# Kernel optimization log

Measured on AMD Instinct MI355X. Metric: run time of the kernel, lower is better.

## Reference

```python
import jax, jax.numpy as jnp
import numpy as np

LOG2 = float(np.log(2.0))

def ssp(x):
    # shifted softplus: log(0.5*exp(x) + 0.5)
    return jax.nn.softplus(x) - LOG2


def setup_inputs() -> dict:
    B, A, N = 8, 512, 64
    n_atom, n_spatial, n_filters = 256, 128, 256
    n_ang_feat = 2 * 2 * 2 * 8 * 2  # 2*n_zetas*2*n_angular*n_zetas = 128
    key = jax.random.key(0)
    ks = jax.random.split(key, 16)
    f32 = jnp.float32
    inp = {
        'x': jax.random.normal(ks[0], (B, A, n_atom), f32),
        'r_ij': jax.random.uniform(ks[1], (B, A, N), f32) * 6.0,  # some beyond cutoff=5
        'f_ij': jax.random.normal(ks[2], (B, A, N, n_spatial), f32),
        'G_i': jax.random.normal(ks[3], (B, A, n_ang_feat), f32),
        'neighbor_mask': jnp.ones((B, A, N), f32),
        'neighbors': jax.random.randint(ks[4], (B, A, N), 0, A),
        # CFConv params: in2f (no bias), filter MLP, f2out
        'W_in2f': jax.random.normal(ks[5], (n_atom, n_filters), f32) * (n_atom ** -0.5),
        'W1': jax.random.normal(ks[6], (n_spatial, n_filters), f32) * (n_spatial ** -0.5),
        'b1': jnp.zeros((n_filters,), f32),
        'W2': jax.random.normal(ks[7], (n_filters, n_filters), f32) * (n_filters ** -0.5),
        'b2': jnp.zeros((n_filters,), f32),
        'W_f2out': jax.random.normal(ks[8], (n_filters, n_atom), f32) * (n_filters ** -0.5),
        'b_f2out': jnp.zeros((n_atom,), f32),
        # post-cfconv dense and angular dense (no bias)
        'W_dense': jax.random.normal(ks[9], (n_atom, n_atom), f32) * (n_atom ** -0.5),
        'b_dense': jnp.zeros((n_atom,), f32),
        'W_ang': jax.random.normal(ks[10], (n_ang_feat, n_atom), f32) * (n_ang_feat ** -0.5),
    }
    return inp


def reference(x, r_ij, f_ij, G_i, neighbor_mask, neighbors,
              W_in2f, W1, b1, W2, b2, W_f2out, b_f2out,
              W_dense, b_dense, W_ang):
    cutoff = 5.0
    # filter-generating MLP on distance expansion: [B,A,N,n_filters]
    W = ssp(jnp.einsum('bans,sf->banf', f_ij, W1) + b1)
    W = jnp.einsum('banf,fg->bang', W, W2) + b2
    # hard cutoff mask on distances
    C = (r_ij <= cutoff).astype(W.dtype)
    W = W * C[..., None]
    # in2f projection then neighbor gather
    xf = jnp.einsum('bad,df->baf', x, W_in2f)  # [B,A,F]
    B, A, F = xf.shape
    N = neighbors.shape[-1]
    y = jnp.take_along_axis(xf, neighbors.reshape(B, A * N, 1), axis=1)
    y = y.reshape(B, A, N, F)
    # elementwise filter, mask padded neighbors, sum-aggregate over neighbors
    y = (y * W * neighbor_mask[..., None]).sum(axis=2)  # [B,A,F]
    v_rad = jnp.einsum('baf,fd->bad', y, W_f2out) + b_f2out
    v_rad = jnp.einsum('bad,de->bae', v_rad, W_dense) + b_dense
    v_ang = jnp.einsum('bag,gd->bad', G_i, W_ang)
    return ssp(v_rad + v_ang)
```

## Files before the change

kernel.cpp:

```cpp
#include <hip/hip_runtime.h>


typedef __bf16 bf16x8 __attribute__((ext_vector_type(8)));
typedef __bf16 bf16x2 __attribute__((ext_vector_type(2)));
typedef float f32x4 __attribute__((ext_vector_type(4)));
typedef int i32x4 __attribute__((ext_vector_type(4)));
typedef unsigned short u16;
typedef unsigned int u32;

#define LDA 136
#define LDH 264

static __device__ __forceinline__ float b2f(u16 u) {
  union { float f; u32 i; } v; v.i = ((u32)u) << 16; return v.f;
}
static __device__ __forceinline__ u16 f2b(float f) {
  return __builtin_bit_cast(u16, (__bf16)f);
}
static __device__ __forceinline__ u32 pk2(float lo, float hi) {
  bf16x2 v; v[0] = (__bf16)lo; v[1] = (__bf16)hi;
  return __builtin_bit_cast(u32, v);
}
static __device__ __forceinline__ float sspf(float x) {
  float t = __expf(fminf(x, 60.0f));
  return __logf(fmaf(t, 0.5f, 0.5f));
}
static __device__ __forceinline__ bf16x8 ldfrag(const u16* p) {
  return __builtin_bit_cast(bf16x8, *(const uint4*)p);
}
static __device__ __forceinline__ float ldsc(const u16* p, bool fm, size_t i) {
  return fm ? ((const float*)p)[i] : b2f(p[i]);
}

static __device__ __forceinline__ void pack_strip(
    const u16* __restrict__ W, bool fm, int q, int KC, u16* __restrict__ dst, u16* T) {
  int tid = threadIdx.x;
  if (fm) {
    const float* src = (const float*)W + (size_t)q * 32 * 256;
#pragma unroll
    for (int i = 0; i < 8; i++) {
      int c = tid + 256 * i;
      int row = c >> 6, col4 = (c & 63) * 4;
      float4 v = *(const float4*)(src + (size_t)row * 256 + col4);
      uint2 o; o.x = pk2(v.x, v.y); o.y = pk2(v.z, v.w);
      *(uint2*)(T + row * LDH + col4) = o;
    }
  } else {
    const u16* src = W + (size_t)q * 32 * 256;
#pragma unroll
    for (int i = 0; i < 8; i++) {
      int c = tid + 256 * i;
      int row = c >> 6, col4 = (c & 63) * 4;
      *(uint2*)(T + row * LDH + col4) = *(const uint2*)(src + (size_t)row * 256 + col4);
    }
  }
  __syncthreads();
#pragma unroll
  for (int i = 0; i < 4; i++) {
    int idx = tid + 256 * i;
    int flane = idx & 63, c = idx >> 6;
    int col = c * 16 + (flane & 15);
    int r0 = (flane >> 4) * 8;
    u32 t0 = (u32)T[(r0 + 0) * LDH + col] | ((u32)T[(r0 + 1) * LDH + col] << 16);
    u32 t1 = (u32)T[(r0 + 2) * LDH + col] | ((u32)T[(r0 + 3) * LDH + col] << 16);
    u32 t2 = (u32)T[(r0 + 4) * LDH + col] | ((u32)T[(r0 + 5) * LDH + col] << 16);
    u32 t3 = (u32)T[(r0 + 6) * LDH + col] | ((u32)T[(r0 + 7) * LDH + col] << 16);
    uint4 o; o.x = t0; o.y = t1; o.z = t2; o.w = t3;
    *(uint4*)(dst + ((size_t)(c * KC + q) * 64 + flane) * 8) = o;
  }
}

__global__ __launch_bounds__(256) void pack_a(
    const u16* __restrict__ Win, const u16* __restrict__ W1, const u16* __restrict__ W2,
    const u16* __restrict__ nm, u16* __restrict__ outb) {
  __shared__ __align__(16) u16 T[32 * LDH];
  bool fm = (nm[0] == 0);
  int b = blockIdx.x;
  if (b < 8)       pack_strip(Win, fm, b,      8, outb + 1048576, T);
  else if (b < 12) pack_strip(W1,  fm, b - 8,  4, outb + 1114112, T);
  else             pack_strip(W2,  fm, b - 12, 8, outb + 1146880, T);
}

__global__ __launch_bounds__(256) void pack_b(
    const u16* __restrict__ Wf, const u16* __restrict__ Wd, const u16* __restrict__ Wa,
    const u16* __restrict__ nm, u16* __restrict__ dst) {
  __shared__ __align__(16) u16 T[32 * LDH];
  bool fm = (nm[0] == 0);
  int b = blockIdx.x;
  if (b < 8)       pack_strip(Wf, fm, b,      8, dst + 98304,  T);
  else if (b < 16) pack_strip(Wd, fm, b - 8,  8, dst + 163840, T);
  else             pack_strip(Wa, fm, b - 16, 4, dst + 229376, T);
}

__global__ __launch_bounds__(256) void k1_xf(
    const u16* __restrict__ x, const u16* __restrict__ nm, u16* __restrict__ outb) {
  __shared__ __align__(16) u16 sX[16 * LDH];
  bool fm = (nm[0] == 0);
  int bid = blockIdx.x, tid = threadIdx.x;
  int w = tid >> 6, lane = tid & 63, quad = lane >> 4, l16 = lane & 15;
  if (fm) {
    const float* src = (const float*)x + (size_t)bid * 4096;
#pragma unroll
    for (int i = 0; i < 2; i++) {
      int c = tid + 256 * i;
      float4 a = *(const float4*)(src + c * 8), b = *(const float4*)(src + c * 8 + 4);
      uint4 o; o.x = pk2(a.x, a.y); o.y = pk2(a.z, a.w);
      o.z = pk2(b.x, b.y); o.w = pk2(b.z, b.w);
      *(uint4*)(sX + (c >> 5) * LDH + (c & 31) * 8) = o;
    }
  } else {
    const u16* src = x + (size_t)bid * 4096;
#pragma unroll
    for (int i = 0; i < 2; i++) {
      int c = tid + 256 * i;
      *(uint4*)(sX + (c >> 5) * LDH + (c & 31) * 8) = *(const uint4*)(src + c * 8);
    }
  }
  __syncthreads();
  const u16* winp = outb + 1048576;
  f32x4 acc[4];
#pragma unroll
  for (int ct = 0; ct < 4; ct++) acc[ct] = (f32x4){0.f, 0.f, 0.f, 0.f};
#pragma unroll
  for (int q = 0; q < 8; q++) {
    bf16x8 af = ldfrag(sX + l16 * LDH + q * 32 + quad * 8);
    bf16x8 bfr[4];
#pragma unroll
    for (int ct = 0; ct < 4; ct++)
      bfr[ct] = ldfrag(winp + ((size_t)((w * 4 + ct) * 8 + q) * 64 + lane) * 8);
#pragma unroll
    for (int ct = 0; ct < 4; ct++)
      acc[ct] = __builtin_amdgcn_mfma_f32_16x16x32_bf16(af, bfr[ct], acc[ct], 0, 0, 0);
  }
#pragma unroll
  for (int ct = 0; ct < 4; ct++) {
    int f = w * 64 + ct * 16 + l16;
#pragma unroll
    for (int r = 0; r < 4; r++)
      outb[(size_t)(bid * 16 + quad * 4 + r) * 256 + f] = f2b(acc[ct][r]);
  }
}

__global__ __launch_bounds__(256, 3) void k2_main(
    u16* __restrict__ fij, const u16* __restrict__ rij, const u16* __restrict__ nm,
    const int* __restrict__ nbr, const u16* __restrict__ b1, const u16* __restrict__ b2,
    const u16* __restrict__ xf) {
  __shared__ __align__(16) u16 sF[64 * LDA];
  __shared__ __align__(16) u16 sH[64 * LDH];
  __shared__ __align__(16) float cm[64];
  __shared__ __align__(16) int nb[64];
  bool fm = (nm[0] == 0);
  const u16* w1p = xf + 1114112;
  const u16* w2p = xf + 1146880;
  int bid = blockIdx.x, tid = threadIdx.x;
  int w = tid >> 6, lane = tid & 63, quad = lane >> 4, l16 = lane & 15;

  if (fm) {
    const float* fsrc = (const float*)fij + (size_t)bid * 8192;
#pragma unroll
    for (int i = 0; i < 4; i++) {
      int c = tid + 256 * i;
      const float* p = fsrc + c * 8;
      float4 a = *(const float4*)p, b = *(const float4*)(p + 4);
      uint4 o; o.x = pk2(a.x, a.y); o.y = pk2(a.z, a.w);
      o.z = pk2(b.x, b.y); o.w = pk2(b.z, b.w);
      *(uint4*)(sF + (c >> 4) * LDA + (c & 15) * 8) = o;
    }
  } else {
    const u16* fsrc = fij + (size_t)bid * 8192;
#pragma unroll
    for (int i = 0; i < 4; i++) {
      int c = tid + 256 * i;
      *(uint4*)(sF + (c >> 4) * LDA + (c & 15) * 8) = *(const uint4*)(fsrc + c * 8);
    }
  }
  if (tid < 64) {
    float r = ldsc(rij, fm, (size_t)bid * 64 + tid);
    float m = ldsc(nm, fm, (size_t)bid * 64 + tid);
    cm[tid] = (r <= 5.0f) ? m : 0.0f;
    nb[tid] = nbr[bid * 64 + tid];
  }
  __syncthreads();

  f32x4 zero = {0.f, 0.f, 0.f, 0.f};
  f32x4 acc[4][4];
#pragma unroll
  for (int mt = 0; mt < 4; mt++)
#pragma unroll
    for (int ct = 0; ct < 4; ct++) acc[mt][ct] = zero;
#pragma unroll
  for (int q = 0; q < 4; q++) {
    bf16x8 af[4], bfr[4];
#pragma unroll
    for (int mt = 0; mt < 4; mt++)
      af[mt] = ldfrag(sF + (mt * 16 + l16) * LDA + q * 32 + quad * 8);
#pragma unroll
    for (int ct = 0; ct < 4; ct++)
      bfr[ct] = ldfrag(w1p + ((size_t)((w * 4 + ct) * 4 + q) * 64 + lane) * 8);
#pragma unroll
    for (int mt = 0; mt < 4; mt++)
#pragma unroll
      for (int ct = 0; ct < 4; ct++)
        acc[mt][ct] = __builtin_amdgcn_mfma_f32_16x16x32_bf16(af[mt], bfr[ct], acc[mt][ct], 0, 0, 0);
  }
  float bb1[4];
#pragma unroll
  for (int ct = 0; ct < 4; ct++) bb1[ct] = ldsc(b1, fm, w * 64 + ct * 16 + l16);
#pragma unroll
  for (int ct = 0; ct < 4; ct++) {
    int f = w * 64 + ct * 16 + l16;
#pragma unroll
    for (int mt = 0; mt < 4; mt++)
#pragma unroll
      for (int r = 0; r < 4; r++)
        sH[(mt * 16 + quad * 4 + r) * LDH + f] = f2b(sspf(acc[mt][ct][r] + bb1[ct]));
  }
  __syncthreads();

  f32x4 acc2[4][4];
#pragma unroll
  for (int mt = 0; mt < 4; mt++)
#pragma unroll
    for (int ct = 0; ct < 4; ct++) acc2[mt][ct] = zero;
#pragma unroll 2
  for (int q = 0; q < 8; q++) {
    bf16x8 af[4], bfr[4];
#pragma unroll
    for (int mt = 0; mt < 4; mt++)
      af[mt] = ldfrag(sH + (mt * 16 + l16) * LDH + q * 32 + quad * 8);
#pragma unroll
    for (int ct = 0; ct < 4; ct++)
      bfr[ct] = ldfrag(w2p + ((size_t)((w * 4 + ct) * 8 + q) * 64 + lane) * 8);
#pragma unroll
    for (int mt = 0; mt < 4; mt++)
#pragma unroll
      for (int ct = 0; ct < 4; ct++)
        acc2[mt][ct] = __builtin_amdgcn_mfma_f32_16x16x32_bf16(af[mt], bfr[ct], acc2[mt][ct], 0, 0, 0);
  }

  float bb2[4];
#pragma unroll
  for (int ct = 0; ct < 4; ct++) bb2[ct] = ldsc(b2, fm, w * 64 + ct * 16 + l16);
  int b_of = (bid >> 9) * 512;
  float s[4] = {0.f, 0.f, 0.f, 0.f};
#pragma unroll
  for (int mt = 0; mt < 4; mt++) {
    f32x4 cmv = *(const f32x4*)(cm + mt * 16 + quad * 4);
    i32x4 nbv = *(const i32x4*)(nb + mt * 16 + quad * 4);
#pragma unroll
    for (int r = 0; r < 4; r++) {
      const u16* xrow = xf + (size_t)(b_of + nbv[r]) * 256 + w * 64 + l16;
      float c = cmv[r];
#pragma unroll
      for (int ct = 0; ct < 4; ct++)
        s[ct] = fmaf((acc2[mt][ct][r] + bb2[ct]) * c, b2f(xrow[ct * 16]), s[ct]);
    }
  }
#pragma unroll
  for (int ct = 0; ct < 4; ct++) {
    s[ct] += __shfl_xor(s[ct], 16);
    s[ct] += __shfl_xor(s[ct], 32);
  }
  if (quad == 0) {
    size_t yoff = (size_t)bid * (fm ? 16384 : 8192);
#pragma unroll
    for (int ct = 0; ct < 4; ct++)
      fij[yoff + w * 64 + ct * 16 + l16] = f2b(s[ct]);
  }
}

__global__ __launch_bounds__(256, 3) void k3_out(
    const u16* __restrict__ fij, const u16* __restrict__ G, const u16* __restrict__ bf2,
    const u16* __restrict__ bd, const u16* __restrict__ nm,
    const u16* __restrict__ packed, u16* __restrict__ outb) {
  __shared__ __align__(16) u16 sY[32 * LDH];
  __shared__ __align__(16) u16 sH2[32 * LDH];
  __shared__ __align__(16) u16 sG[32 * LDA];
  bool fm = (nm[0] == 0);
  const u16* wfp = packed + 98304;
  const u16* wdp = packed + 163840;
  const u16* wap = packed + 229376;
  int bid = blockIdx.x, tid = threadIdx.x;
  int w = tid >> 6, lane = tid & 63, quad = lane >> 4, l16 = lane & 15;
  size_t ystr = fm ? 16384 : 8192;
#pragma unroll
  for (int i = 0; i < 4; i++) {
    int c = tid + 256 * i;
    int row = c >> 5;
    const u16* src = fij + (size_t)(bid * 32 + row) * ystr + (c & 31) * 8;
    *(uint4*)(sY + row * LDH + (c & 31) * 8) = *(const uint4*)src;
  }
  if (fm) {
    const float* g32 = (const float*)G;
#pragma unroll
    for (int i = 0; i < 2; i++) {
      int c = tid + 256 * i;
      int row = c >> 4;
      const float* p = g32 + (size_t)(bid * 32 + row) * 128 + (c & 15) * 8;
      float4 a = *(const float4*)p, b = *(const float4*)(p + 4);
      uint4 o; o.x = pk2(a.x, a.y); o.y = pk2(a.z, a.w);
      o.z = pk2(b.x, b.y); o.w = pk2(b.z, b.w);
      *(uint4*)(sG + row * LDA + (c & 15) * 8) = o;
    }
  } else {
#pragma unroll
    for (int i = 0; i < 2; i++) {
      int c = tid + 256 * i;
      int row = c >> 4;
      *(uint4*)(sG + row * LDA + (c & 15) * 8) =
          *(const uint4*)(G + (size_t)(bid * 32 + row) * 128 + (c & 15) * 8);
    }
  }
  __syncthreads();
  f32x4 zero = {0.f, 0.f, 0.f, 0.f};
  f32x4 acc[2][4];
#pragma unroll
  for (int mt = 0; mt < 2; mt++)
#pragma unroll
    for (int ct = 0; ct < 4; ct++) acc[mt][ct] = zero;
#pragma unroll
  for (int q = 0; q < 8; q++) {
    bf16x8 af[2], bfr[4];
#pragma unroll
    for (int mt = 0; mt < 2; mt++)
      af[mt] = ldfrag(sY + (mt * 16 + l16) * LDH + q * 32 + quad * 8);
#pragma unroll
    for (int ct = 0; ct < 4; ct++)
      bfr[ct] = ldfrag(wfp + ((size_t)((w * 4 + ct) * 8 + q) * 64 + lane) * 8);
#pragma unroll
    for (int mt = 0; mt < 2; mt++)
#pragma unroll
      for (int ct = 0; ct < 4; ct++)
        acc[mt][ct] = __builtin_amdgcn_mfma_f32_16x16x32_bf16(af[mt], bfr[ct], acc[mt][ct], 0, 0, 0);
  }
#pragma unroll
  for (int ct = 0; ct < 4; ct++) {
    int f = w * 64 + ct * 16 + l16;
    float bb = ldsc(bf2, fm, f);
#pragma unroll
    for (int mt = 0; mt < 2; mt++)
#pragma unroll
      for (int r = 0; r < 4; r++)
        sH2[(mt * 16 + quad * 4 + r) * LDH + f] = f2b(acc[mt][ct][r] + bb);
  }
  __syncthreads();
#pragma unroll
  for (int mt = 0; mt < 2; mt++)
#pragma unroll
    for (int ct = 0; ct < 4; ct++) acc[mt][ct] = zero;
#pragma unroll
  for (int q = 0; q < 8; q++) {
    bf16x8 af[2], bfr[4];
#pragma unroll
    for (int mt = 0; mt < 2; mt++)
      af[mt] = ldfrag(sH2 + (mt * 16 + l16) * LDH + q * 32 + quad * 8);
#pragma unroll
    for (int ct = 0; ct < 4; ct++)
      bfr[ct] = ldfrag(wdp + ((size_t)((w * 4 + ct) * 8 + q) * 64 + lane) * 8);
#pragma unroll
    for (int mt = 0; mt < 2; mt++)
#pragma unroll
      for (int ct = 0; ct < 4; ct++)
        acc[mt][ct] = __builtin_amdgcn_mfma_f32_16x16x32_bf16(af[mt], bfr[ct], acc[mt][ct], 0, 0, 0);
  }
#pragma unroll
  for (int q = 0; q < 4; q++) {
    bf16x8 af[2], bfr[4];
#pragma unroll
    for (int mt = 0; mt < 2; mt++)
      af[mt] = ldfrag(sG + (mt * 16 + l16) * LDA + q * 32 + quad * 8);
#pragma unroll
    for (int ct = 0; ct < 4; ct++)
      bfr[ct] = ldfrag(wap + ((size_t)((w * 4 + ct) * 4 + q) * 64 + lane) * 8);
#pragma unroll
    for (int mt = 0; mt < 2; mt++)
#pragma unroll
      for (int ct = 0; ct < 4; ct++)
        acc[mt][ct] = __builtin_amdgcn_mfma_f32_16x16x32_bf16(af[mt], bfr[ct], acc[mt][ct], 0, 0, 0);
  }
  float* out32 = (float*)outb;
#pragma unroll
  for (int ct = 0; ct < 4; ct++) {
    int f = w * 64 + ct * 16 + l16;
    float bb = ldsc(bd, fm, f);
#pragma unroll
    for (int mt = 0; mt < 2; mt++)
#pragma unroll
      for (int r = 0; r < 4; r++) {
        int m = mt * 16 + quad * 4 + r;
        float v = sspf(acc[mt][ct][r] + bb);
        size_t idx = ((size_t)bid * 32 + m) * 256 + f;
        if (fm) out32[idx] = v; else outb[idx] = f2b(v);
      }
  }
}

extern "C" void kernel_launch(void* const* d_in, const int* in_sizes, int n_in,
                              void* d_out, int out_size, void* d_ws, size_t ws_size,
                              hipStream_t stream) {
  u16*       x    = (u16*)d_in[0];
  const u16* rij  = (const u16*)d_in[1];
  u16*       fij  = (u16*)d_in[2];
  const u16* Gi   = (const u16*)d_in[3];
  const u16* nmsk = (const u16*)d_in[4];
  const int* nbr  = (const int*)d_in[5];
  const u16* Win  = (const u16*)d_in[6];
  const u16* W1   = (const u16*)d_in[7];
  const u16* b1   = (const u16*)d_in[8];
  const u16* W2   = (const u16*)d_in[9];
  const u16* b2   = (const u16*)d_in[10];
  const u16* Wf   = (const u16*)d_in[11];
  const u16* bf2  = (const u16*)d_in[12];
  const u16* Wd   = (const u16*)d_in[13];
  const u16* bd   = (const u16*)d_in[14];
  const u16* Wa   = (const u16*)d_in[15];
  u16* out = (u16*)d_out;

  pack_a<<<20, 256, 0, stream>>>(Win, W1, W2, nmsk, out);
  k1_xf<<<256, 256, 0, stream>>>(x, nmsk, out);
  pack_b<<<20, 256, 0, stream>>>(Wf, Wd, Wa, nmsk, x);
  k2_main<<<4096, 256, 0, stream>>>(fij, rij, nmsk, nbr, b1, b2, out);
  k3_out<<<128, 256, 0, stream>>>(fij, Gi, bf2, bd, nmsk, x, out);
}
```

Baseline: 293.6 us.

## Permute packed weight columns for vectorized stores and gathers; alias LDS; retile k1/k3

Packed weight fragments now use a column permutation, so each lane owns four adjacent output features. Epilogues can then write packed uint2 stores, and the neighbor gather of xf loads 8 bytes at once instead of four scalar bf16 loads. k2 aliases the f_ij and hidden LDS buffers to cut shared memory and raises the occupancy hint to 4 blocks. An extra barrier is added to make the aliasing safe. k1 and k3 are retiled into smaller row blocks with more blocks and threads for better parallelism.

```diff
diff --git a/kernel.cpp b/kernel.cpp
--- a/kernel.cpp
+++ b/kernel.cpp
@@ -14,6 +14,12 @@
 static __device__ __forceinline__ float b2f(u16 u) {
   union { float f; u32 i; } v; v.i = ((u32)u) << 16; return v.f;
 }
+static __device__ __forceinline__ float b2f_lo(u32 p) {
+  union { float f; u32 i; } v; v.i = p << 16; return v.f;
+}
+static __device__ __forceinline__ float b2f_hi(u32 p) {
+  union { float f; u32 i; } v; v.i = p & 0xffff0000u; return v.f;
+}
 static __device__ __forceinline__ u16 f2b(float f) {
   return __builtin_bit_cast(u16, (__bf16)f);
 }
@@ -59,7 +65,7 @@
   for (int i = 0; i < 4; i++) {
     int idx = tid + 256 * i;
     int flane = idx & 63, c = idx >> 6;
-    int col = c * 16 + (flane & 15);
+    int col = (c >> 2) * 64 + (flane & 15) * 4 + (c & 3);
     int r0 = (flane >> 4) * 8;
     u32 t0 = (u32)T[(r0 + 0) * LDH + col] | ((u32)T[(r0 + 1) * LDH + col] << 16);
     u32 t1 = (u32)T[(r0 + 2) * LDH + col] | ((u32)T[(r0 + 3) * LDH + col] << 16);
@@ -99,22 +105,16 @@
   int bid = blockIdx.x, tid = threadIdx.x;
   int w = tid >> 6, lane = tid & 63, quad = lane >> 4, l16 = lane & 15;
   if (fm) {
-    const float* src = (const float*)x + (size_t)bid * 4096;
-#pragma unroll
-    for (int i = 0; i < 2; i++) {
-      int c = tid + 256 * i;
-      float4 a = *(const float4*)(src + c * 8), b = *(const float4*)(src + c * 8 + 4);
-      uint4 o; o.x = pk2(a.x, a.y); o.y = pk2(a.z, a.w);
-      o.z = pk2(b.x, b.y); o.w = pk2(b.z, b.w);
-      *(uint4*)(sX + (c >> 5) * LDH + (c & 31) * 8) = o;
-    }
-  } else {
-    const u16* src = x + (size_t)bid * 4096;
-#pragma unroll
-    for (int i = 0; i < 2; i++) {
-      int c = tid + 256 * i;
-      *(uint4*)(sX + (c >> 5) * LDH + (c & 31) * 8) = *(const uint4*)(src + c * 8);
-    }
+    const float* src = (const float*)x + (size_t)bid * 2048;
+    int c = tid;
+    float4 a = *(const float4*)(src + c * 8), b = *(const float4*)(src + c * 8 + 4);
+    uint4 o; o.x = pk2(a.x, a.y); o.y = pk2(a.z, a.w);
+    o.z = pk2(b.x, b.y); o.w = pk2(b.z, b.w);
+    *(uint4*)(sX + (c >> 5) * LDH + (c & 31) * 8) = o;
+  } else {
+    const u16* src = x + (size_t)bid * 2048;
+    int c = tid;
+    *(uint4*)(sX + (c >> 5) * LDH + (c & 31) * 8) = *(const uint4*)(src + c * 8);
   }
   __syncthreads();
   const u16* winp = outb + 1048576;
@@ -132,26 +132,28 @@
     for (int ct = 0; ct < 4; ct++)
       acc[ct] = __builtin_amdgcn_mfma_f32_16x16x32_bf16(af, bfr[ct], acc[ct], 0, 0, 0);
   }
-#pragma unroll
-  for (int ct = 0; ct < 4; ct++) {
-    int f = w * 64 + ct * 16 + l16;
-#pragma unroll
-    for (int r = 0; r < 4; r++)
-      outb[(size_t)(bid * 16 + quad * 4 + r) * 256 + f] = f2b(acc[ct][r]);
-  }
-}
-
-__global__ __launch_bounds__(256, 3) void k2_main(
+  if (quad < 2) {
+#pragma unroll
+    for (int r = 0; r < 4; r++) {
+      uint2 o; o.x = pk2(acc[0][r], acc[1][r]); o.y = pk2(acc[2][r], acc[3][r]);
+      *(uint2*)(outb + (size_t)(bid * 8 + quad * 4 + r) * 256 + w * 64 + l16 * 4) = o;
+    }
+  }
+}
+
+__global__ __launch_bounds__(256, 4) void k2_main(
     u16* __restrict__ fij, const u16* __restrict__ rij, const u16* __restrict__ nm,
     const int* __restrict__ nbr, const u16* __restrict__ b1, const u16* __restrict__ b2,
-    const u16* __restrict__ xf) {
-  __shared__ __align__(16) u16 sF[64 * LDA];
-  __shared__ __align__(16) u16 sH[64 * LDH];
+    const u16* __restrict__ outb) {
+  __shared__ __align__(16) u16 sU[64 * LDH];
   __shared__ __align__(16) float cm[64];
   __shared__ __align__(16) int nb[64];
+  u16* sF = sU;
+  u16* sH = sU;
   bool fm = (nm[0] == 0);
-  const u16* w1p = xf + 1114112;
-  const u16* w2p = xf + 1146880;
+  const u16* xf  = outb;
+  const u16* w1p = outb + 1114112;
+  const u16* w2p = outb + 1146880;
   int bid = blockIdx.x, tid = threadIdx.x;
   int w = tid >> 6, lane = tid & 63, quad = lane >> 4, l16 = lane & 15;
 
@@ -203,18 +205,26 @@
       for (int ct = 0; ct < 4; ct++)
         acc[mt][ct] = __builtin_amdgcn_mfma_f32_16x16x32_bf16(af[mt], bfr[ct], acc[mt][ct], 0, 0, 0);
   }
+  __syncthreads();
+
   float bb1[4];
-#pragma unroll
-  for (int ct = 0; ct < 4; ct++) bb1[ct] = ldsc(b1, fm, w * 64 + ct * 16 + l16);
-#pragma unroll
-  for (int ct = 0; ct < 4; ct++) {
-    int f = w * 64 + ct * 16 + l16;
-#pragma unroll
-    for (int mt = 0; mt < 4; mt++)
-#pragma unroll
-      for (int r = 0; r < 4; r++)
-        sH[(mt * 16 + quad * 4 + r) * LDH + f] = f2b(sspf(acc[mt][ct][r] + bb1[ct]));
-  }
+  if (fm) {
+    float4 t = *(const float4*)((const float*)b1 + w * 64 + l16 * 4);
+    bb1[0] = t.x; bb1[1] = t.y; bb1[2] = t.z; bb1[3] = t.w;
+  } else {
+    uint2 t = *(const uint2*)(b1 + w * 64 + l16 * 4);
+    bb1[0] = b2f_lo(t.x); bb1[1] = b2f_hi(t.x); bb1[2] = b2f_lo(t.y); bb1[3] = b2f_hi(t.y);
+  }
+#pragma unroll
+  for (int mt = 0; mt < 4; mt++)
+#pragma unroll
+    for (int r = 0; r < 4; r++) {
+      int m = mt * 16 + quad * 4 + r;
+      uint2 o;
+      o.x = pk2(sspf(acc[mt][0][r] + bb1[0]), sspf(acc[mt][1][r] + bb1[1]));
+      o.y = pk2(sspf(acc[mt][2][r] + bb1[2]), sspf(acc[mt][3][r] + bb1[3]));
+      *(uint2*)(sH + m * LDH + w * 64 + l16 * 4) = o;
+    }
   __syncthreads();
 
   f32x4 acc2[4][4];
@@ -239,159 +249,149 @@
   }
 
   float bb2[4];
-#pragma unroll
-  for (int ct = 0; ct < 4; ct++) bb2[ct] = ldsc(b2, fm, w * 64 + ct * 16 + l16);
+  if (fm) {
+    float4 t = *(const float4*)((const float*)b2 + w * 64 + l16 * 4);
+    bb2[0] = t.x; bb2[1] = t.y; bb2[2] = t.z; bb2[3] = t.w;
+  } else {
+    uint2 t = *(const uint2*)(b2 + w * 64 + l16 * 4);
+    bb2[0] = b2f_lo(t.x); bb2[1] = b2f_hi(t.x); bb2[2] = b2f_lo(t.y); bb2[3] = b2f_hi(t.y);
+  }
   int b_of = (bid >> 9) * 512;
-  float s[4] = {0.f, 0.f, 0.f, 0.f};
+  const u16* xcol = xf + w * 64 + l16 * 4;
+  float s0 = 0.f, s1 = 0.f, s2 = 0.f, s3 = 0.f;
 #pragma unroll
   for (int mt = 0; mt < 4; mt++) {
     f32x4 cmv = *(const f32x4*)(cm + mt * 16 + quad * 4);
     i32x4 nbv = *(const i32x4*)(nb + mt * 16 + quad * 4);
 #pragma unroll
     for (int r = 0; r < 4; r++) {
-      const u16* xrow = xf + (size_t)(b_of + nbv[r]) * 256 + w * 64 + l16;
+      uint2 xv = *(const uint2*)(xcol + (size_t)(b_of + nbv[r]) * 256);
       float c = cmv[r];
-#pragma unroll
-      for (int ct = 0; ct < 4; ct++)
-        s[ct] = fmaf((acc2[mt][ct][r] + bb2[ct]) * c, b2f(xrow[ct * 16]), s[ct]);
-    }
-  }
-#pragma unroll
-  for (int ct = 0; ct < 4; ct++) {
-    s[ct] += __shfl_xor(s[ct], 16);
-    s[ct] += __shfl_xor(s[ct], 32);
-  }
+      s0 = fmaf((acc2[mt][0][r] + bb2[0]) * c, b2f_lo(xv.x), s0);
+      s1 = fmaf((acc2[mt][1][r] + bb2[1]) * c, b2f_hi(xv.x), s1);
+      s2 = fmaf((acc2[mt][2][r] + bb2[2]) * c, b2f_lo(xv.y), s2);
+      s3 = fmaf((acc2[mt][3][r] + bb2[3]) * c, b2f_hi(xv.y), s3);
+    }
+  }
+  s0 += __shfl_xor(s0, 16); s0 += __shfl_xor(s0, 32);
+  s1 += __shfl_xor(s1, 16); s1 += __shfl_xor(s1, 32);
+  s2 += __shfl_xor(s2, 16); s2 += __shfl_xor(s2, 32);
+  s3 += __shfl_xor(s3, 16); s3 += __shfl_xor(s3, 32);
   if (quad == 0) {
     size_t yoff = (size_t)bid * (fm ? 16384 : 8192);
-#pragma unroll
-    for (int ct = 0; ct < 4; ct++)
-      fij[yoff + w * 64 + ct * 16 + l16] = f2b(s[ct]);
-  }
-}
-
-__global__ __launch_bounds__(256, 3) void k3_out(
+    uint2 o; o.x = pk2(s0, s1); o.y = pk2(s2, s3);
+    *(uint2*)(fij + yoff + w * 64 + l16 * 4) = o;
+  }
+}
+
+__global__ __launch_bounds__(512) void k3_out(
     const u16* __restrict__ fij, const u16* __restrict__ G, const u16* __restrict__ bf2,
     const u16* __restrict__ bd, const u16* __restrict__ nm,
     const u16* __restrict__ packed, u16* __restrict__ outb) {
-  __shared__ __align__(16) u16 sY[32 * LDH];
-  __shared__ __align__(16) u16 sH2[32 * LDH];
-  __shared__ __align__(16) u16 sG[32 * LDA];
+  __shared__ __align__(16) u16 sY[16 * LDH];
+  __shared__ __align__(16) u16 sH2[16 * LDH];
+  __shared__ __align__(16) u16 sG[16 * LDA];
   bool fm = (nm[0] == 0);
   const u16* wfp = packed + 98304;
   const u16* wdp = packed + 163840;
   const u16* wap = packed + 229376;
   int bid = blockIdx.x, tid = threadIdx.x;
-  int w = tid >> 6, lane = tid & 63, quad = lane >> 4, l16 = lane & 15;
+  int cg = tid >> 6, lane = tid & 63, quad = lane >> 4, l16 = lane & 15;
+  int f0 = (cg >> 1) * 64 + l16 * 4 + (cg & 1) * 2;
   size_t ystr = fm ? 16384 : 8192;
-#pragma unroll
-  for (int i = 0; i < 4; i++) {
-    int c = tid + 256 * i;
-    int row = c >> 5;
-    const u16* src = fij + (size_t)(bid * 32 + row) * ystr + (c & 31) * 8;
-    *(uint4*)(sY + row * LDH + (c & 31) * 8) = *(const uint4*)src;
-  }
-  if (fm) {
-    const float* g32 = (const float*)G;
-#pragma unroll
-    for (int i = 0; i < 2; i++) {
-      int c = tid + 256 * i;
-      int row = c >> 4;
-      const float* p = g32 + (size_t)(bid * 32 + row) * 128 + (c & 15) * 8;
+  {
+    int c = tid;
+    const u16* src = fij + (size_t)(bid * 16 + (c >> 5)) * ystr + (c & 31) * 8;
+    *(uint4*)(sY + (c >> 5) * LDH + (c & 31) * 8) = *(const uint4*)src;
+  }
+  if (fm) {
+    if (tid < 256) {
+      int c = tid;
+      const float* p = (const float*)G + (size_t)(bid * 16 + (c >> 4)) * 128 + (c & 15) * 8;
       float4 a = *(const float4*)p, b = *(const float4*)(p + 4);
       uint4 o; o.x = pk2(a.x, a.y); o.y = pk2(a.z, a.w);
       o.z = pk2(b.x, b.y); o.w = pk2(b.z, b.w);
-      *(uint4*)(sG + row * LDA + (c & 15) * 8) = o;
-    }
-  } else {
-#pragma unroll
-    for (int i = 0; i < 2; i++) {
-      int c = tid + 256 * i;
-      int row = c >> 4;
-      *(uint4*)(sG + row * LDA + (c & 15) * 8) =
-          *(const uint4*)(G + (size_t)(bid * 32 + row) * 128 + (c & 15) * 8);
+      *(uint4*)(sG + (c >> 4) * LDA + (c & 15) * 8) = o;
+    }
+  } else {
+    if (tid < 256) {
+      int c = tid;
+      *(uint4*)(sG + (c >> 4) * LDA + (c & 15) * 8) =
+          *(const uint4*)(G + (size_t)(bid * 16 + (c >> 4)) * 128 + (c & 15) * 8);
     }
   }
   __syncthreads();
   f32x4 zero = {0.f, 0.f, 0.f, 0.f};
-  f32x4 acc[2][4];
-#pragma unroll
-  for (int mt = 0; mt < 2; mt++)
-#pragma unroll
-    for (int ct = 0; ct < 4; ct++) acc[mt][ct] = zero;
+  f32x4 acc[2];
+  acc[0] = zero; acc[1] = zero;
 #pragma unroll
   for (int q = 0; q < 8; q++) {
-    bf16x8 af[2], bfr[4];
-#pragma unroll
-    for (int mt = 0; mt < 2; mt++)
-      af[mt] = ldfrag(sY + (mt * 16 + l16) * LDH + q * 32 + quad * 8);
-#pragma unroll
-    for (int ct = 0; ct < 4; ct++)
-      bfr[ct] = ldfrag(wfp + ((size_t)((w * 4 + ct) * 8 + q) * 64 + lane) * 8);
-#pragma unroll
-    for (int mt = 0; mt < 2; mt++)
-#pragma unroll
-      for (int ct = 0; ct < 4; ct++)
-        acc[mt][ct] = __builtin_amdgcn_mfma_f32_16x16x32_bf16(af[mt], bfr[ct], acc[mt][ct], 0, 0, 0);
-  }
-#pragma unroll
-  for (int ct = 0; ct < 4; ct++) {
-    int f = w * 64 + ct * 16 + l16;
-    float bb = ldsc(bf2, fm, f);
-#pragma unroll
-    for (int mt = 0; mt < 2; mt++)
-#pragma unroll
-      for (int r = 0; r < 4; r++)
-        sH2[(mt * 16 + quad * 4 + r) * LDH + f] = f2b(acc[mt][ct][r] + bb);
-  }
-  __syncthreads();
-#pragma unroll
-  for (int mt = 0; mt < 2; mt++)
-#pragma unroll
-    for (int ct = 0; ct < 4; ct++) acc[mt][ct] = zero;
+    bf16x8 af = ldfrag(sY + l16 * LDH + q * 32 + quad * 8);
+    bf16x8 bfr[2];
+#pragma unroll
+    for (int ct = 0; ct < 2; ct++)
+      bfr[ct] = ldfrag(wfp + ((size_t)((cg * 2 + ct) * 8 + q) * 64 + lane) * 8);
+#pragma unroll
+    for (int ct = 0; ct < 2; ct++)
+      acc[ct] = __builtin_amdgcn_mfma_f32_16x16x32_bf16(af, bfr[ct], acc[ct], 0, 0, 0);
+  }
+  float bm0, bm1;
+  if (fm) {
+    float2 t = *(const float2*)((const float*)bf2 + f0);
+    bm0 = t.x; bm1 = t.y;
+  } else {
+    u32 t = *(const u32*)(bf2 + f0);
+    bm0 = b2f_lo(t); bm1 = b2f_hi(t);
+  }
+#pragma unroll
+  for (int r = 0; r < 4; r++) {
+    int m = quad * 4 + r;
+    *(u32*)(sH2 + m * LDH + f0) = pk2(acc[0][r] + bm0, acc[1][r] + bm1);
+  }
+  __syncthreads();
+  acc[0] = zero; acc[1] = zero;
 #pragma unroll
   for (int q = 0; q < 8; q++) {
-    bf16x8 af[2], bfr[4];
-#pragma unroll
-    for (int mt = 0; mt < 2; mt++)
-      af[mt] = ldfrag(sH2 + (mt * 16 + l16) * LDH + q * 32 + quad * 8);
-#pragma unroll
-    for (int ct = 0; ct < 4; ct++)
-      bfr[ct] = ldfrag(wdp + ((size_t)((w * 4 + ct) * 8 + q) * 64 + lane) * 8);
-#pragma unroll
-    for (int mt = 0; mt < 2; mt++)
-#pragma unroll
-      for (int ct = 0; ct < 4; ct++)
-        acc[mt][ct] = __builtin_amdgcn_mfma_f32_16x16x32_bf16(af[mt], bfr[ct], acc[mt][ct], 0, 0, 0);
+    bf16x8 af = ldfrag(sH2 + l16 * LDH + q * 32 + quad * 8);
+    bf16x8 bfr[2];
+#pragma unroll
+    for (int ct = 0; ct < 2; ct++)
+      bfr[ct] = ldfrag(wdp + ((size_t)((cg * 2 + ct) * 8 + q) * 64 + lane) * 8);
+#pragma unroll
+    for (int ct = 0; ct < 2; ct++)
+      acc[ct] = __builtin_amdgcn_mfma_f32_16x16x32_bf16(af, bfr[ct], acc[ct], 0, 0, 0);
   }
 #pragma unroll
   for (int q = 0; q < 4; q++) {
-    bf16x8 af[2], bfr[4];
-#pragma unroll
-    for (int mt = 0; mt < 2; mt++)
-      af[mt] = ldfrag(sG + (mt * 16 + l16) * LDA + q * 32 + quad * 8);
-#pragma unroll
-    for (int ct = 0; ct < 4; ct++)
-      bfr[ct] = ldfrag(wap + ((size_t)((w * 4 + ct) * 4 + q) * 64 + lane) * 8);
-#pragma unroll
-    for (int mt = 0; mt < 2; mt++)
-#pragma unroll
-      for (int ct = 0; ct < 4; ct++)
-        acc[mt][ct] = __builtin_amdgcn_mfma_f32_16x16x32_bf16(af[mt], bfr[ct], acc[mt][ct], 0, 0, 0);
+    bf16x8 af = ldfrag(sG + l16 * LDA + q * 32 + quad * 8);
+    bf16x8 bfr[2];
+#pragma unroll
+    for (int ct = 0; ct < 2; ct++)
+      bfr[ct] = ldfrag(wap + ((size_t)((cg * 2 + ct) * 4 + q) * 64 + lane) * 8);
+#pragma unroll
+    for (int ct = 0; ct < 2; ct++)
+      acc[ct] = __builtin_amdgcn_mfma_f32_16x16x32_bf16(af, bfr[ct], acc[ct], 0, 0, 0);
+  }
+  float bd0, bd1;
+  if (fm) {
+    float2 t = *(const float2*)((const float*)bd + f0);
+    bd0 = t.x; bd1 = t.y;
+  } else {
+    u32 t = *(const u32*)(bd + f0);
+    bd0 = b2f_lo(t); bd1 = b2f_hi(t);
   }
   float* out32 = (float*)outb;
 #pragma unroll
-  for (int ct = 0; ct < 4; ct++) {
-    int f = w * 64 + ct * 16 + l16;
-    float bb = ldsc(bd, fm, f);
-#pragma unroll
-    for (int mt = 0; mt < 2; mt++)
-#pragma unroll
-      for (int r = 0; r < 4; r++) {
-        int m = mt * 16 + quad * 4 + r;
-        float v = sspf(acc[mt][ct][r] + bb);
-        size_t idx = ((size_t)bid * 32 + m) * 256 + f;
-        if (fm) out32[idx] = v; else outb[idx] = f2b(v);
-      }
+  for (int r = 0; r < 4; r++) {
+    size_t row = (size_t)bid * 16 + quad * 4 + r;
+    float v0 = sspf(acc[0][r] + bd0);
+    float v1 = sspf(acc[1][r] + bd1);
+    if (fm) {
+      float2 o; o.x = v0; o.y = v1;
+      *(float2*)(out32 + row * 256 + f0) = o;
+    } else {
+      *(u32*)(outb + row * 256 + f0) = pk2(v0, v1);
+    }
   }
 }
 
@@ -417,8 +417,8 @@
   u16* out = (u16*)d_out;
 
   pack_a<<<20, 256, 0, stream>>>(Win, W1, W2, nmsk, out);
-  k1_xf<<<256, 256, 0, stream>>>(x, nmsk, out);
+  k1_xf<<<512, 256, 0, stream>>>(x, nmsk, out);
   pack_b<<<20, 256, 0, stream>>>(Wf, Wd, Wa, nmsk, x);
   k2_main<<<4096, 256, 0, stream>>>(fij, rij, nmsk, nbr, b1, b2, out);
-  k3_out<<<128, 256, 0, stream>>>(fij, Gi, bf2, bd, nmsk, x, out);
-}
+  k3_out<<<256, 512, 0, stream>>>(fij, Gi, bf2, bd, nmsk, x, out);
+}
```

Result: faster. 287.7 us (-2.0%).
